# Optimization experiments

Measured on AMD Instinct MI355X. Metric: run time of the kernel, lower is better.

## Reference

```python
import jax, jax.numpy as jnp
import numpy as np
from jax.scipy.linalg import solve_triangular

B, N = 8192, 1024  # patch batch, neighborhood size; order=3 -> 10 jet coefficients


def setup_inputs() -> dict:
    key = jax.random.key(0)
    k1, k2 = jax.random.split(key)
    points = jax.random.normal(k1, (B, 3, N), dtype=jnp.float32)
    weights = jax.random.uniform(k2, (B, N), dtype=jnp.float32)
    return {"points": points, "weights": weights}


def fit_wjet_order3(points, weights):
    # points: [B,3,N], weights: [B,N]
    bsz, _, n = points.shape
    x = points[:, 0, :, None]  # [B,N,1]
    y = points[:, 1, :, None]
    z = points[:, 2, :, None]
    w = weights[:, :, None]                      # [B,N,1]
    valid_count = jnp.sum(w > 0.001, axis=1)     # [B,1]
    w_vec = jnp.where(valid_count > 18, weights, jnp.ones_like(weights))[:, :, None]  # [B,N,1]

    # scale normalization h (order > 1 branch)
    h = (jnp.mean(jnp.abs(x), axis=1) + jnp.mean(jnp.abs(y), axis=1)) / 2.0  # [B,1]
    h = jnp.where(jnp.abs(h) < 0.0001, 0.1, h)
    hh = h[:, :, None]                            # [B,1,1]
    x = x / hh
    y = y / hh

    # order-3 polynomial feature matrix A: [B,N,10]
    x_2 = x * x
    y_2 = y * y
    xy = x * y
    A = jnp.concatenate([x, y, x_2, y_2, xy, x_2 * x, y_2 * y, x_2 * y, y_2 * x,
                         jnp.ones_like(x)], axis=2)
    h_2 = h * h
    h_3 = h_2 * h
    d_inv = 1.0 / jnp.concatenate([h, h, h_2, h_2, h_2, h_3, h_3, h_3, h_3,
                                   jnp.ones_like(h)], axis=1)  # [B,10]

    # normal equations (weighted): XtX [B,10,10], XtY [B,10,1]
    XtX = jnp.einsum('bnm,bnk->bmk', A, w_vec * A)
    XtY = jnp.einsum('bnm,bnk->bmk', A, w_vec * z)

    # batched Cholesky solve (happy path of solve_linear_system)
    L = jnp.linalg.cholesky(XtX)
    u = solve_triangular(L, XtY, lower=True)
    beta = solve_triangular(jnp.swapaxes(L, -1, -2), u, lower=False)  # [B,10,1]

    beta = d_inv[:, :, None] * beta  # D_inv @ beta (D_inv is diagonal)

    ones_b1 = jnp.ones((bsz, 1), dtype=beta.dtype)
    n_est = jnp.concatenate([-beta[:, 0:2, 0], ones_b1], axis=1)
    n_est = n_est / jnp.linalg.norm(n_est, axis=1, keepdims=True)

    # analytic neighbor normals (order == 3)
    def bk(k):
        return beta[:, k][:, None, :]  # [B,1,1] broadcasts over N
    nx = -(bk(0) + 2 * bk(2) * x + bk(4) * y + 3 * bk(5) * x_2 + 2 * bk(7) * xy + bk(8) * y_2)
    ny = -(bk(1) + 2 * bk(3) * y + bk(4) * x + 3 * bk(6) * y_2 + bk(7) * x_2 + 2 * bk(8) * xy)
    nn_ = jnp.concatenate([nx, ny, jnp.ones((bsz, n, 1), dtype=beta.dtype)], axis=2)  # [B,N,3]
    neighbor_normals = nn_ / jnp.linalg.norm(nn_, axis=2, keepdims=True)

    return beta[:, :, 0], n_est, neighbor_normals


def reference(points, weights):
    return fit_wjet_order3(points, weights)
```

## Files before the change

kernel.cpp:

```cpp
#include <hip/hip_runtime.h>
#include <math.h>

#define NPTS 1024
#define THREADS 256

typedef float v2f __attribute__((ext_vector_type(2)));
typedef int v2i __attribute__((ext_vector_type(2)));

static __device__ __forceinline__ v2f b2(float s) { return (v2f){s, s}; }
static __device__ __forceinline__ v2f vabs2(v2f v) {
  v2i u = __builtin_bit_cast(v2i, v);
  u &= (v2i){0x7fffffff, 0x7fffffff};
  return __builtin_bit_cast(v2f, u);
}

template <int CTRL>
__device__ __forceinline__ float dpp_add(float v) {
  int m = __builtin_amdgcn_update_dpp(0, __builtin_bit_cast(int, v), CTRL, 0xF, 0xF, true);
  return v + __builtin_bit_cast(float, m);
}

__device__ __forceinline__ float row_red16(float v) {
  v = dpp_add<0x111>(v);
  v = dpp_add<0x112>(v);
  v = dpp_add<0x114>(v);
  v = dpp_add<0x118>(v);
  return v;
}

__device__ __forceinline__ float rl_f32(float v, int l) {
  return __builtin_bit_cast(float,
      __builtin_amdgcn_readlane(__builtin_bit_cast(int, v), l));
}

__device__ __forceinline__ float bperm_f(int srclane, float v) {
  return __builtin_bit_cast(float,
      __builtin_amdgcn_ds_bpermute(srclane << 2, __builtin_bit_cast(int, v)));
}

__device__ __forceinline__ float fast_rsq(float x) {
#if __has_builtin(__builtin_amdgcn_rsqf)
  return __builtin_amdgcn_rsqf(x);
#else
  return 1.0f / sqrtf(x);
#endif
}

__device__ __forceinline__ float rcp_nr(float d) {
#if __has_builtin(__builtin_amdgcn_rcpf)
  float r = __builtin_amdgcn_rcpf(d);
  return r * (2.0f - d * r);
#else
  return 1.0f / d;
#endif
}

__global__ void __launch_bounds__(THREADS) deepfit_kernel(
    const float* __restrict__ pts, const float* __restrict__ wts,
    float* __restrict__ beta_out, float* __restrict__ nest_out,
    float* __restrict__ nn_out)
{
  const int b = blockIdx.x;
  const int t = threadIdx.x;
  const int lane = t & 63;
  const int wid = t >> 6;

  __shared__ float s_red[16][40];
  __shared__ int s_cnt[4];
  __shared__ float s_Lf[4][100];
  float* sL = &s_Lf[wid][0];

  const float4* px4 = reinterpret_cast<const float4*>(pts + (size_t)b * (3 * NPTS));
  const float4* pw4 = reinterpret_cast<const float4*>(wts + (size_t)b * NPTS);

  float4 lx4 = px4[t];
  float4 ly4 = px4[THREADS + t];
  float4 lz4 = px4[2 * THREADS + t];
  float4 lw4 = pw4[t];

  v2f xp[2] = {{lx4.x, lx4.y}, {lx4.z, lx4.w}};
  v2f yq[2] = {{ly4.x, ly4.y}, {ly4.z, ly4.w}};
  v2f zp[2] = {{lz4.x, lz4.y}, {lz4.z, lz4.w}};
  v2f wp[2] = {{lw4.x, lw4.y}, {lw4.z, lw4.w}};

  const int part = wid * 4 + (lane >> 4);

  v2f hab2 = vabs2(xp[0]) + vabs2(yq[0]) + vabs2(xp[1]) + vabs2(yq[1]);
  int cnt = 0;
  cnt += (int)__popcll(__ballot(lw4.x > 0.001f));
  cnt += (int)__popcll(__ballot(lw4.y > 0.001f));
  cnt += (int)__popcll(__ballot(lw4.z > 0.001f));
  cnt += (int)__popcll(__ballot(lw4.w > 0.001f));
  {
    float habs = row_red16(hab2.x + hab2.y);
    if ((lane & 15) == 15) s_red[part][39] = habs;
    if (lane == 0) s_cnt[wid] = cnt;
  }

  float momvec = 0.f;
  float mh = 0.1f;
  bool wone = false;
  for (int it = 0; it < 2; ++it) {
    if (it == 1) __syncthreads();
    v2f M2[28], Z2[10];
#pragma unroll
    for (int i = 0; i < 28; ++i) M2[i] = b2(0.f);
#pragma unroll
    for (int i = 0; i < 10; ++i) Z2[i] = b2(0.f);

#pragma unroll
    for (int q = 0; q < 2; ++q) {
      v2f x = xp[q], y = yq[q];
      v2f w = wone ? b2(1.0f) : wp[q];
      v2f wz = w * zp[q];
      v2f y1 = y, y2 = y * y, y3 = y2 * y, y4 = y3 * y, y5 = y4 * y, y6 = y5 * y;
      v2f tx = w;
      M2[0] += tx;          M2[1] += tx * y1; M2[2] += tx * y2; M2[3] += tx * y3;
      M2[4] += tx * y4;     M2[5] += tx * y5; M2[6] += tx * y6;
      tx *= x;
      M2[7] += tx;          M2[8] += tx * y1; M2[9] += tx * y2; M2[10] += tx * y3;
      M2[11] += tx * y4;    M2[12] += tx * y5;
      tx *= x;
      M2[13] += tx;         M2[14] += tx * y1; M2[15] += tx * y2; M2[16] += tx * y3;
      M2[17] += tx * y4;
      tx *= x;
      M2[18] += tx;         M2[19] += tx * y1; M2[20] += tx * y2; M2[21] += tx * y3;
      tx *= x;
      M2[22] += tx;         M2[23] += tx * y1; M2[24] += tx * y2;
      tx *= x;
      M2[25] += tx;         M2[26] += tx * y1;
      tx *= x;
      M2[27] += tx;
      v2f tz = wz;
      Z2[0] += tz;          Z2[1] += tz * y1; Z2[2] += tz * y2; Z2[3] += tz * y3;
      tz *= x;
      Z2[4] += tz;          Z2[5] += tz * y1; Z2[6] += tz * y2;
      tz *= x;
      Z2[7] += tz;          Z2[8] += tz * y1;
      tz *= x;
      Z2[9] += tz;
    }

#pragma unroll
    for (int i = 0; i < 28; ++i) {
      float v = row_red16(M2[i].x + M2[i].y);
      if ((lane & 15) == 15) s_red[part][i] = v;
    }
#pragma unroll
    for (int i = 0; i < 10; ++i) {
      float v = row_red16(Z2[i].x + Z2[i].y);
      if ((lane & 15) == 15) s_red[part][28 + i] = v;
    }
    __syncthreads();

    float acc = 0.f;
    if (lane < 40) {
#pragma unroll
      for (int j = 0; j < 16; ++j) acc += s_red[j][lane];
    }
    momvec = acc;
    {
      float htot = rl_f32(momvec, 39);
      mh = htot * (1.0f / 2048.0f);
      if (fabsf(mh) < 1e-4f) mh = 0.1f;
    }
    int ctot = s_cnt[0] + s_cnt[1] + s_cnt[2] + s_cnt[3];
    if (it == 1 || ctot > 18) break;
    wone = true;
  }

  const int lc = (lane < 10) ? lane : 0;
  const int axi = (0x18D21u >> (2 * lc)) & 3;
  const int ayi = (0x27184u >> (2 * lc)) & 3;
  constexpr int AXC[10] = {1, 0, 2, 0, 1, 3, 0, 2, 1, 0};
  constexpr int AYC[10] = {0, 1, 0, 2, 1, 0, 3, 1, 2, 0};
  float a[10], yy;
#pragma unroll
  for (int j = 0; j < 10; ++j) {
    int as = axi + AXC[j];
    int bs = ayi + AYC[j];
    int idx = as * 7 - (as * (as - 1)) / 2 + bs;
    a[j] = bperm_f(idx, momvec);
  }
  {
    int zi = axi * 4 - (axi * (axi - 1)) / 2 + ayi;
    yy = bperm_f(28 + zi, momvec);
  }

  float bf = 0.f;
  if (lane < 10) {
    float rd_own = 1.0f;
#pragma unroll
    for (int j = 0; j < 10; ++j) {
      float dj = rl_f32(a[j], j);
      float rdj = rcp_nr(dj);
      float lij = a[j] * rdj;
      sL[lane * 10 + j] = lij;
      if (lane == j) rd_own = rdj;
      float wj = rl_f32(yy, j);
      if (lane > j) yy -= lij * wj;
#pragma unroll
      for (int k = j + 1; k < 10; ++k) {
        float ajk = rl_f32(a[k], j);
        a[k] -= lij * ajk;
      }
    }
    yy *= rd_own;
    asm volatile("s_waitcnt lgkmcnt(0)" ::: "memory");
    __builtin_amdgcn_sched_barrier(0);
#pragma unroll
    for (int j = 9; j >= 0; --j) {
      float xj = rl_f32(yy, j);
      if (lane < j) yy -= sL[j * 10 + lane] * xj;
    }
    bf = yy;
    if (wid == 0) beta_out[(size_t)b * 10 + lane] = bf;
  }

  float bb[10];
#pragma unroll
  for (int j = 0; j < 10; ++j) bb[j] = rl_f32(bf, j);
  if (wid == 0 && lane == 0) {
    float b0 = bb[0], b1 = bb[1];
    float invn = fast_rsq(b0 * b0 + b1 * b1 + 1.0f);
    nest_out[(size_t)b * 3 + 0] = -b0 * invn;
    nest_out[(size_t)b * 3 + 1] = -b1 * invn;
    nest_out[(size_t)b * 3 + 2] = invn;
  }
  const float ih = 1.0f / mh;
  const float ih2 = ih * ih;
  const float u0 = bb[0], u2 = 2.f * bb[2] * ih, u4 = bb[4] * ih;
  const float u5 = 3.f * bb[5] * ih2, u7 = 2.f * bb[7] * ih2, u8 = bb[8] * ih2;
  const float v1 = bb[1], v3 = 2.f * bb[3] * ih, v4 = bb[4] * ih;
  const float v6 = 3.f * bb[6] * ih2, v7 = bb[7] * ih2, v8 = 2.f * bb[8] * ih2;

  float nx[4], ny[4], nz[4];
#pragma unroll
  for (int q = 0; q < 2; ++q) {
    v2f x = xp[q], y = yq[q];
    v2f x2 = x * x, y2 = y * y, xy = x * y;
    v2f sx = b2(u0) + b2(u2) * x + b2(u4) * y + b2(u5) * x2 + b2(u7) * xy + b2(u8) * y2;
    v2f sy = b2(v1) + b2(v3) * y + b2(v4) * x + b2(v6) * y2 + b2(v7) * x2 + b2(v8) * xy;
    v2f vx = -sx, vy = -sy;
    v2f n2 = vx * vx + vy * vy + b2(1.0f);
    float i0 = fast_rsq(n2.x), i1 = fast_rsq(n2.y);
    nx[2 * q + 0] = vx.x * i0; ny[2 * q + 0] = vy.x * i0; nz[2 * q + 0] = i0;
    nx[2 * q + 1] = vx.y * i1; ny[2 * q + 1] = vy.y * i1; nz[2 * q + 1] = i1;
  }
  {
    float4* o4 = reinterpret_cast<float4*>(nn_out + (size_t)b * (NPTS * 3));
    float4 f0 = make_float4(nx[0], ny[0], nz[0], nx[1]);
    float4 f1 = make_float4(ny[1], nz[1], nx[2], ny[2]);
    float4 f2 = make_float4(nz[2], nx[3], ny[3], nz[3]);
    o4[3 * t + 0] = f0;
    o4[3 * t + 1] = f1;
    o4[3 * t + 2] = f2;
  }
}

extern "C" void kernel_launch(void* const* d_in, const int* in_sizes, int n_in,
                              void* d_out, int out_size, void* d_ws, size_t ws_size,
                              hipStream_t stream) {
  const float* pts = (const float*)d_in[0];
  const float* wts = (const float*)d_in[1];
  float* out = (float*)d_out;
  const int B = in_sizes[1] / NPTS;
  float* beta_out = out;
  float* nest_out = out + (size_t)B * 10;
  float* nn_out = out + (size_t)B * 13;
  deepfit_kernel<<<B, THREADS, 0, stream>>>(pts, wts, beta_out, nest_out, nn_out);
}
```

Before: 52.21 us.

## Assign one wavefront per patch and drop block-wide barriers

Each patch is now handled by a single 64-lane wavefront that walks all 1024 points in four chunks, with four patches per block. This removes the cross-wave __syncthreads reductions and the redundant Cholesky solve that every wave used to repeat. The unit-weight fallback becomes a conditional second pass that reloads z and reuses the cached x/y chunks. The cost is more registers per lane for the cached x/y and accumulators, and each wave has a longer serial accumulation loop.

```diff
diff --git a/kernel.cpp b/kernel.cpp
--- a/kernel.cpp
+++ b/kernel.cpp
@@ -2,7 +2,8 @@
 #include <math.h>
 
 #define NPTS 1024
-#define THREADS 256
+#define WPB 4
+#define THREADS (64 * WPB)
 
 typedef float v2f __attribute__((ext_vector_type(2)));
 typedef int v2i __attribute__((ext_vector_type(2)));
@@ -55,118 +56,126 @@
 #endif
 }
 
+__device__ __forceinline__ void acc_pair(v2f M2[28], v2f Z2[10],
+                                         v2f x, v2f y, v2f w, v2f z) {
+  v2f wz = w * z;
+  v2f y1 = y, y2 = y * y, y3 = y2 * y, y4 = y3 * y, y5 = y4 * y, y6 = y5 * y;
+  v2f tx = w;
+  M2[0] += tx;          M2[1] += tx * y1; M2[2] += tx * y2; M2[3] += tx * y3;
+  M2[4] += tx * y4;     M2[5] += tx * y5; M2[6] += tx * y6;
+  tx *= x;
+  M2[7] += tx;          M2[8] += tx * y1; M2[9] += tx * y2; M2[10] += tx * y3;
+  M2[11] += tx * y4;    M2[12] += tx * y5;
+  tx *= x;
+  M2[13] += tx;         M2[14] += tx * y1; M2[15] += tx * y2; M2[16] += tx * y3;
+  M2[17] += tx * y4;
+  tx *= x;
+  M2[18] += tx;         M2[19] += tx * y1; M2[20] += tx * y2; M2[21] += tx * y3;
+  tx *= x;
+  M2[22] += tx;         M2[23] += tx * y1; M2[24] += tx * y2;
+  tx *= x;
+  M2[25] += tx;         M2[26] += tx * y1;
+  tx *= x;
+  M2[27] += tx;
+  v2f tz = wz;
+  Z2[0] += tz;          Z2[1] += tz * y1; Z2[2] += tz * y2; Z2[3] += tz * y3;
+  tz *= x;
+  Z2[4] += tz;          Z2[5] += tz * y1; Z2[6] += tz * y2;
+  tz *= x;
+  Z2[7] += tz;          Z2[8] += tz * y1;
+  tz *= x;
+  Z2[9] += tz;
+}
+
 __global__ void __launch_bounds__(THREADS) deepfit_kernel(
     const float* __restrict__ pts, const float* __restrict__ wts,
     float* __restrict__ beta_out, float* __restrict__ nest_out,
-    float* __restrict__ nn_out)
+    float* __restrict__ nn_out, int B)
 {
-  const int b = blockIdx.x;
-  const int t = threadIdx.x;
-  const int lane = t & 63;
-  const int wid = t >> 6;
-
-  __shared__ float s_red[16][40];
-  __shared__ int s_cnt[4];
-  __shared__ float s_Lf[4][100];
+  const int lane = threadIdx.x & 63;
+  const int wid = threadIdx.x >> 6;
+  const int b = blockIdx.x * WPB + wid;
+  if (b >= B) return;
+
+  __shared__ float s_part[WPB][4][40];
+  __shared__ float s_Lf[WPB][100];
   float* sL = &s_Lf[wid][0];
 
   const float4* px4 = reinterpret_cast<const float4*>(pts + (size_t)b * (3 * NPTS));
   const float4* pw4 = reinterpret_cast<const float4*>(wts + (size_t)b * NPTS);
 
-  float4 lx4 = px4[t];
-  float4 ly4 = px4[THREADS + t];
-  float4 lz4 = px4[2 * THREADS + t];
-  float4 lw4 = pw4[t];
-
-  v2f xp[2] = {{lx4.x, lx4.y}, {lx4.z, lx4.w}};
-  v2f yq[2] = {{ly4.x, ly4.y}, {ly4.z, ly4.w}};
-  v2f zp[2] = {{lz4.x, lz4.y}, {lz4.z, lz4.w}};
-  v2f wp[2] = {{lw4.x, lw4.y}, {lw4.z, lw4.w}};
-
-  const int part = wid * 4 + (lane >> 4);
-
-  v2f hab2 = vabs2(xp[0]) + vabs2(yq[0]) + vabs2(xp[1]) + vabs2(yq[1]);
+  float4 xc[4], yc[4];
+  v2f M2[28], Z2[10];
+#pragma unroll
+  for (int i = 0; i < 28; ++i) M2[i] = b2(0.f);
+#pragma unroll
+  for (int i = 0; i < 10; ++i) Z2[i] = b2(0.f);
+  v2f hab2 = b2(0.f);
   int cnt = 0;
-  cnt += (int)__popcll(__ballot(lw4.x > 0.001f));
-  cnt += (int)__popcll(__ballot(lw4.y > 0.001f));
-  cnt += (int)__popcll(__ballot(lw4.z > 0.001f));
-  cnt += (int)__popcll(__ballot(lw4.w > 0.001f));
+
+#pragma unroll
+  for (int c = 0; c < 4; ++c) {
+    xc[c] = px4[lane + 64 * c];
+    yc[c] = px4[256 + lane + 64 * c];
+    float4 z4 = px4[512 + lane + 64 * c];
+    float4 w4 = pw4[lane + 64 * c];
+    v2f xq[2] = {{xc[c].x, xc[c].y}, {xc[c].z, xc[c].w}};
+    v2f yq[2] = {{yc[c].x, yc[c].y}, {yc[c].z, yc[c].w}};
+    v2f zq[2] = {{z4.x, z4.y}, {z4.z, z4.w}};
+    v2f wq[2] = {{w4.x, w4.y}, {w4.z, w4.w}};
+    cnt += (int)__popcll(__ballot(w4.x > 0.001f));
+    cnt += (int)__popcll(__ballot(w4.y > 0.001f));
+    cnt += (int)__popcll(__ballot(w4.z > 0.001f));
+    cnt += (int)__popcll(__ballot(w4.w > 0.001f));
+#pragma unroll
+    for (int q = 0; q < 2; ++q) {
+      hab2 += vabs2(xq[q]) + vabs2(yq[q]);
+      acc_pair(M2, Z2, xq[q], yq[q], wq[q], zq[q]);
+    }
+  }
+
+  if (cnt <= 18) {
+#pragma unroll
+    for (int i = 0; i < 28; ++i) M2[i] = b2(0.f);
+#pragma unroll
+    for (int i = 0; i < 10; ++i) Z2[i] = b2(0.f);
+    for (int c = 0; c < 4; ++c) {
+      float4 z4 = px4[512 + lane + 64 * c];
+      v2f xq[2] = {{xc[c].x, xc[c].y}, {xc[c].z, xc[c].w}};
+      v2f yq[2] = {{yc[c].x, yc[c].y}, {yc[c].z, yc[c].w}};
+      v2f zq[2] = {{z4.x, z4.y}, {z4.z, z4.w}};
+#pragma unroll
+      for (int q = 0; q < 2; ++q)
+        acc_pair(M2, Z2, xq[q], yq[q], b2(1.0f), zq[q]);
+    }
+  }
+
+  const int grp = lane >> 4;
+  const bool gw = ((lane & 15) == 15);
+#pragma unroll
+  for (int i = 0; i < 28; ++i) {
+    float v = row_red16(M2[i].x + M2[i].y);
+    if (gw) s_part[wid][grp][i] = v;
+  }
+#pragma unroll
+  for (int i = 0; i < 10; ++i) {
+    float v = row_red16(Z2[i].x + Z2[i].y);
+    if (gw) s_part[wid][grp][28 + i] = v;
+  }
   {
-    float habs = row_red16(hab2.x + hab2.y);
-    if ((lane & 15) == 15) s_red[part][39] = habs;
-    if (lane == 0) s_cnt[wid] = cnt;
-  }
-
+    float v = row_red16(hab2.x + hab2.y);
+    if (gw) s_part[wid][grp][38] = v;
+  }
   float momvec = 0.f;
-  float mh = 0.1f;
-  bool wone = false;
-  for (int it = 0; it < 2; ++it) {
-    if (it == 1) __syncthreads();
-    v2f M2[28], Z2[10];
-#pragma unroll
-    for (int i = 0; i < 28; ++i) M2[i] = b2(0.f);
-#pragma unroll
-    for (int i = 0; i < 10; ++i) Z2[i] = b2(0.f);
-
-#pragma unroll
-    for (int q = 0; q < 2; ++q) {
-      v2f x = xp[q], y = yq[q];
-      v2f w = wone ? b2(1.0f) : wp[q];
-      v2f wz = w * zp[q];
-      v2f y1 = y, y2 = y * y, y3 = y2 * y, y4 = y3 * y, y5 = y4 * y, y6 = y5 * y;
-      v2f tx = w;
-      M2[0] += tx;          M2[1] += tx * y1; M2[2] += tx * y2; M2[3] += tx * y3;
-      M2[4] += tx * y4;     M2[5] += tx * y5; M2[6] += tx * y6;
-      tx *= x;
-      M2[7] += tx;          M2[8] += tx * y1; M2[9] += tx * y2; M2[10] += tx * y3;
-      M2[11] += tx * y4;    M2[12] += tx * y5;
-      tx *= x;
-      M2[13] += tx;         M2[14] += tx * y1; M2[15] += tx * y2; M2[16] += tx * y3;
-      M2[17] += tx * y4;
-      tx *= x;
-      M2[18] += tx;         M2[19] += tx * y1; M2[20] += tx * y2; M2[21] += tx * y3;
-      tx *= x;
-      M2[22] += tx;         M2[23] += tx * y1; M2[24] += tx * y2;
-      tx *= x;
-      M2[25] += tx;         M2[26] += tx * y1;
-      tx *= x;
-      M2[27] += tx;
-      v2f tz = wz;
-      Z2[0] += tz;          Z2[1] += tz * y1; Z2[2] += tz * y2; Z2[3] += tz * y3;
-      tz *= x;
-      Z2[4] += tz;          Z2[5] += tz * y1; Z2[6] += tz * y2;
-      tz *= x;
-      Z2[7] += tz;          Z2[8] += tz * y1;
-      tz *= x;
-      Z2[9] += tz;
-    }
-
-#pragma unroll
-    for (int i = 0; i < 28; ++i) {
-      float v = row_red16(M2[i].x + M2[i].y);
-      if ((lane & 15) == 15) s_red[part][i] = v;
-    }
-#pragma unroll
-    for (int i = 0; i < 10; ++i) {
-      float v = row_red16(Z2[i].x + Z2[i].y);
-      if ((lane & 15) == 15) s_red[part][28 + i] = v;
-    }
-    __syncthreads();
-
-    float acc = 0.f;
-    if (lane < 40) {
-#pragma unroll
-      for (int j = 0; j < 16; ++j) acc += s_red[j][lane];
-    }
-    momvec = acc;
-    {
-      float htot = rl_f32(momvec, 39);
-      mh = htot * (1.0f / 2048.0f);
-      if (fabsf(mh) < 1e-4f) mh = 0.1f;
-    }
-    int ctot = s_cnt[0] + s_cnt[1] + s_cnt[2] + s_cnt[3];
-    if (it == 1 || ctot > 18) break;
-    wone = true;
+  if (lane < 39)
+    momvec = (s_part[wid][0][lane] + s_part[wid][1][lane]) +
+             (s_part[wid][2][lane] + s_part[wid][3][lane]);
+
+  float mh;
+  {
+    float htot = rl_f32(momvec, 38);
+    mh = htot * (1.0f / 2048.0f);
+    if (fabsf(mh) < 1e-4f) mh = 0.1f;
   }
 
   const int lc = (lane < 10) ? lane : 0;
@@ -214,13 +223,13 @@
       if (lane < j) yy -= sL[j * 10 + lane] * xj;
     }
     bf = yy;
-    if (wid == 0) beta_out[(size_t)b * 10 + lane] = bf;
+    beta_out[(size_t)b * 10 + lane] = bf;
   }
 
   float bb[10];
 #pragma unroll
   for (int j = 0; j < 10; ++j) bb[j] = rl_f32(bf, j);
-  if (wid == 0 && lane == 0) {
+  if (lane == 0) {
     float b0 = bb[0], b1 = bb[1];
     float invn = fast_rsq(b0 * b0 + b1 * b1 + 1.0f);
     nest_out[(size_t)b * 3 + 0] = -b0 * invn;
@@ -234,27 +243,28 @@
   const float v1 = bb[1], v3 = 2.f * bb[3] * ih, v4 = bb[4] * ih;
   const float v6 = 3.f * bb[6] * ih2, v7 = bb[7] * ih2, v8 = 2.f * bb[8] * ih2;
 
-  float nx[4], ny[4], nz[4];
-#pragma unroll
-  for (int q = 0; q < 2; ++q) {
-    v2f x = xp[q], y = yq[q];
-    v2f x2 = x * x, y2 = y * y, xy = x * y;
-    v2f sx = b2(u0) + b2(u2) * x + b2(u4) * y + b2(u5) * x2 + b2(u7) * xy + b2(u8) * y2;
-    v2f sy = b2(v1) + b2(v3) * y + b2(v4) * x + b2(v6) * y2 + b2(v7) * x2 + b2(v8) * xy;
-    v2f vx = -sx, vy = -sy;
-    v2f n2 = vx * vx + vy * vy + b2(1.0f);
-    float i0 = fast_rsq(n2.x), i1 = fast_rsq(n2.y);
-    nx[2 * q + 0] = vx.x * i0; ny[2 * q + 0] = vy.x * i0; nz[2 * q + 0] = i0;
-    nx[2 * q + 1] = vx.y * i1; ny[2 * q + 1] = vy.y * i1; nz[2 * q + 1] = i1;
-  }
-  {
-    float4* o4 = reinterpret_cast<float4*>(nn_out + (size_t)b * (NPTS * 3));
-    float4 f0 = make_float4(nx[0], ny[0], nz[0], nx[1]);
-    float4 f1 = make_float4(ny[1], nz[1], nx[2], ny[2]);
-    float4 f2 = make_float4(nz[2], nx[3], ny[3], nz[3]);
-    o4[3 * t + 0] = f0;
-    o4[3 * t + 1] = f1;
-    o4[3 * t + 2] = f2;
+  float4* o4 = reinterpret_cast<float4*>(nn_out + (size_t)b * (NPTS * 3));
+#pragma unroll
+  for (int c = 0; c < 4; ++c) {
+    v2f xq[2] = {{xc[c].x, xc[c].y}, {xc[c].z, xc[c].w}};
+    v2f yq[2] = {{yc[c].x, yc[c].y}, {yc[c].z, yc[c].w}};
+    float nx[4], ny[4], nz[4];
+#pragma unroll
+    for (int q = 0; q < 2; ++q) {
+      v2f x = xq[q], y = yq[q];
+      v2f x2 = x * x, y2 = y * y, xy = x * y;
+      v2f sx = b2(u0) + b2(u2) * x + b2(u4) * y + b2(u5) * x2 + b2(u7) * xy + b2(u8) * y2;
+      v2f sy = b2(v1) + b2(v3) * y + b2(v4) * x + b2(v6) * y2 + b2(v7) * x2 + b2(v8) * xy;
+      v2f vx = -sx, vy = -sy;
+      v2f n2 = vx * vx + vy * vy + b2(1.0f);
+      float i0 = fast_rsq(n2.x), i1 = fast_rsq(n2.y);
+      nx[2 * q + 0] = vx.x * i0; ny[2 * q + 0] = vy.x * i0; nz[2 * q + 0] = i0;
+      nx[2 * q + 1] = vx.y * i1; ny[2 * q + 1] = vy.y * i1; nz[2 * q + 1] = i1;
+    }
+    int base = 3 * (lane + 64 * c);
+    o4[base + 0] = make_float4(nx[0], ny[0], nz[0], nx[1]);
+    o4[base + 1] = make_float4(ny[1], nz[1], nx[2], ny[2]);
+    o4[base + 2] = make_float4(nz[2], nx[3], ny[3], nz[3]);
   }
 }
 
@@ -268,5 +278,6 @@
   float* beta_out = out;
   float* nest_out = out + (size_t)B * 10;
   float* nn_out = out + (size_t)B * 13;
-  deepfit_kernel<<<B, THREADS, 0, stream>>>(pts, wts, beta_out, nest_out, nn_out);
-}
+  const int grid = (B + WPB - 1) / WPB;
+  deepfit_kernel<<<grid, THREADS, 0, stream>>>(pts, wts, beta_out, nest_out, nn_out, B);
+}
```

Result: no change. 52.46 us (+0.5%).
